# Kernel tuning notes

Hardware: AMD Instinct MI355X
Metric: run time of the kernel (lower is better)

The kernel has to match this reference:

```python
import jax, jax.numpy as jnp
import numpy as np

D = 128; H = 8; L = 6; DFF = 512; EPS = 1e-5; ETA = 1e-3; MAXLEN = 5000


def layernorm(x, g, b):
    m = jnp.mean(x, -1, keepdims=True)
    v = jnp.mean((x - m) ** 2, -1, keepdims=True)
    return (x - m) / jnp.sqrt(v + EPS) * g + b


def mha(q_in, kv_in, Wi, bi, Wo, bo):
    # Wi: [3D, D] packed q/k/v projections (torch in_proj layout)
    dh = D // H
    q = q_in @ Wi[:D].T + bi[:D]
    k = kv_in @ Wi[D:2 * D].T + bi[D:2 * D]
    v = kv_in @ Wi[2 * D:].T + bi[2 * D:]
    B_, Lq, _ = q.shape
    Lk = k.shape[1]
    q = q.reshape(B_, Lq, H, dh)
    k = k.reshape(B_, Lk, H, dh)
    v = v.reshape(B_, Lk, H, dh)
    att = jax.nn.softmax(jnp.einsum('bqhd,bkhd->bhqk', q, k) / jnp.sqrt(jnp.asarray(dh, q.dtype)), axis=-1)
    o = jnp.einsum('bhqk,bkhd->bqhd', att, v).reshape(B_, Lq, D)
    return o @ Wo.T + bo


def posenc(x):
    pos = jnp.arange(MAXLEN, dtype=x.dtype)[:, None]
    div = jnp.exp(jnp.arange(0, D, 2, dtype=x.dtype) * (-jnp.log(jnp.asarray(10000.0, x.dtype)) / D))
    pe = jnp.zeros((MAXLEN, D), x.dtype).at[:, 0::2].set(jnp.sin(pos * div)).at[:, 1::2].set(jnp.cos(pos * div))
    # faithful to original: slices pe by x.size(0) which is the BATCH dim (batch_first tensors)
    return x + pe[: x.shape[0], None, :]


def reference(src, tgt, emb, femb_w, femb_b,
              enc_inw, enc_inb, enc_ow, enc_ob, enc_l1g, enc_l1b, enc_l2g, enc_l2b,
              enc_f1w, enc_f1b, enc_f2w, enc_f2b, enc_ng, enc_nb,
              dec_inw, dec_inb, dec_ow, dec_ob, dec_cinw, dec_cinb, dec_cow, dec_cob,
              dec_l1g, dec_l1b, dec_l2g, dec_l2b, dec_l3g, dec_l3b,
              dec_f1w, dec_f1b, dec_f2w, dec_f2b, dec_ng, dec_nb, fc_w, fc_b):
    scale = jnp.sqrt(jnp.asarray(D, jnp.float32))
    s = posenc(emb[src] * scale)                     # [B,S,D]
    t = posenc((tgt @ femb_w.T + femb_b) * scale)    # [B,T,D]
    mem = s
    for i in range(L):  # encoder (post-norm, ReLU, dropout=0 in eval)
        a = mha(mem, mem, enc_inw[i], enc_inb[i], enc_ow[i], enc_ob[i])
        mem = layernorm(mem + a, enc_l1g[i], enc_l1b[i])
        f = jax.nn.relu(mem @ enc_f1w[i].T + enc_f1b[i]) @ enc_f2w[i].T + enc_f2b[i]
        mem = layernorm(mem + f, enc_l2g[i], enc_l2b[i])
    mem = layernorm(mem, enc_ng, enc_nb)
    y = t
    for i in range(L):  # decoder
        a = mha(y, y, dec_inw[i], dec_inb[i], dec_ow[i], dec_ob[i])
        y = layernorm(y + a, dec_l1g[i], dec_l1b[i])
        c = mha(y, mem, dec_cinw[i], dec_cinb[i], dec_cow[i], dec_cob[i])
        y = layernorm(y + c, dec_l2g[i], dec_l2b[i])
        f = jax.nn.relu(y @ dec_f1w[i].T + dec_f1b[i]) @ dec_f2w[i].T + dec_f2b[i]
        y = layernorm(y + f, dec_l3g[i], dec_l3b[i])
    y = layernorm(y, dec_ng, dec_nb)
    out = y @ fc_w.T + fc_b  # [B,T,1]
    # nn-corrected TN parameter vector: vec + eta * nn_output (pre-final-contract)
    return tgt[..., 0] + ETA * out[..., 0]


def setup_inputs():
    B, S, T = 4, 100, 2048
    ks = iter(jax.random.split(jax.random.key(0), 64))

    def w(shape, s=0.02):
        return jax.random.normal(next(ks), shape, jnp.float32) * s

    inp = {}
    inp['src'] = jax.random.randint(next(ks), (B, S), 0, 2)
    inp['tgt'] = jax.random.normal(next(ks), (B, T, 1), jnp.float32)
    inp['emb'] = w((2, D), 1.0)
    inp['femb_w'] = w((D, 1)); inp['femb_b'] = jnp.zeros((D,))
    inp['enc_inw'] = w((L, 3 * D, D)); inp['enc_inb'] = jnp.zeros((L, 3 * D))
    inp['enc_ow'] = w((L, D, D)); inp['enc_ob'] = jnp.zeros((L, D))
    inp['enc_l1g'] = jnp.ones((L, D)); inp['enc_l1b'] = jnp.zeros((L, D))
    inp['enc_l2g'] = jnp.ones((L, D)); inp['enc_l2b'] = jnp.zeros((L, D))
    inp['enc_f1w'] = w((L, DFF, D)); inp['enc_f1b'] = jnp.zeros((L, DFF))
    inp['enc_f2w'] = w((L, D, DFF)); inp['enc_f2b'] = jnp.zeros((L, D))
    inp['enc_ng'] = jnp.ones((D,)); inp['enc_nb'] = jnp.zeros((D,))
    inp['dec_inw'] = w((L, 3 * D, D)); inp['dec_inb'] = jnp.zeros((L, 3 * D))
    inp['dec_ow'] = w((L, D, D)); inp['dec_ob'] = jnp.zeros((L, D))
    inp['dec_cinw'] = w((L, 3 * D, D)); inp['dec_cinb'] = jnp.zeros((L, 3 * D))
    inp['dec_cow'] = w((L, D, D)); inp['dec_cob'] = jnp.zeros((L, D))
    inp['dec_l1g'] = jnp.ones((L, D)); inp['dec_l1b'] = jnp.zeros((L, D))
    inp['dec_l2g'] = jnp.ones((L, D)); inp['dec_l2b'] = jnp.zeros((L, D))
    inp['dec_l3g'] = jnp.ones((L, D)); inp['dec_l3b'] = jnp.zeros((L, D))
    inp['dec_f1w'] = w((L, DFF, D)); inp['dec_f1b'] = jnp.zeros((L, DFF))
    inp['dec_f2w'] = w((L, D, DFF)); inp['dec_f2b'] = jnp.zeros((L, D))
    inp['dec_ng'] = jnp.ones((D,)); inp['dec_nb'] = jnp.zeros((D,))
    inp['fc_w'] = w((1, D)); inp['fc_b'] = jnp.zeros((1,))
    return inp
```

## Files before the change

### kernel.cpp

```cpp
#include <hip/hip_runtime.h>
#include <hip/hip_bf16.h>
#include <math.h>

#define B_ 4
#define S_ 100
#define T_ 2048
#define DM 128
#define NH 8
#define DH 16
#define NL 6
#define DFFN 512

#define SQRT_D 11.313708498984761f
#define LN10K  9.210340371976184f
#define QSCALE 0.36067376022224085f

typedef _Float16 v4h __attribute__((ext_vector_type(4)));
typedef _Float16 v8h __attribute__((ext_vector_type(8)));
typedef float    v4f __attribute__((ext_vector_type(4)));

__device__ __forceinline__ float fexp2(float x) { return __builtin_amdgcn_exp2f(x); }

__device__ __forceinline__ v4f mfma16(v4h a, v4h b, v4f c) {
    return __builtin_amdgcn_mfma_f32_16x16x16f16(a, b, c, 0, 0, 0);
// ... 95 lines not shown
    v4f acc[4][2];
    #pragma unroll
    for (int m = 0; m < 4; m++)
        #pragma unroll
        for (int n = 0; n < 2; n++) acc[m][n] = (v4f){0.f, 0.f, 0.f, 0.f};

    for (int k0 = 0; k0 < K; k0 += 64) {
        #pragma unroll
        for (int i = 0; i < 4; i++) {
            int id = i * 256 + t;
            int r = id >> 3, j = id & 7;
            int gr = min(row0 + r, M - 1);
            int4 v = *(const int4*)(A + (size_t)gr * K + k0 + j * 8);
            *(int4*)&As[r][j * 8] = v;
        }
        #pragma unroll
        for (int i = 0; i < 2; i++) {
            int id = i * 256 + t;
            int r = id >> 3, j = id & 7;
            int4 v = *(const int4*)(W + (size_t)(col0 + r) * K + k0 + j * 8);
            *(int4*)&Ws[r][j * 8] = v;
        }
        __syncthreads();
        #pragma unroll
        for (int kk = 0; kk < 4; kk++) {
            v4h a[4], bf[2];
            #pragma unroll
            for (int m = 0; m < 4; m++)
                a[m] = *(const v4h*)&As[wrow0 + m * 16 + col16][kk * 16 + grp * 4];
            #pragma unroll
            for (int n = 0; n < 2; n++)
                bf[n] = *(const v4h*)&Ws[wcol0 + n * 16 + col16][kk * 16 + grp * 4];
            #pragma unroll
            for (int m = 0; m < 4; m++)
                #pragma unroll
                for (int n = 0; n < 2; n++)
                    acc[m][n] = mfma16(a[m], bf[n], acc[m][n]);
        }
        __syncthreads();
    }

    #pragma unroll
    for (int n = 0; n < 2; n++) {
        int gcol = col0 + wcol0 + n * 16 + col16;
        float bv = bias[gcol];
        #pragma unroll
        for (int m = 0; m < 4; m++) {
            int rbase = row0 + wrow0 + m * 16 + grp * 4;
            #pragma unroll
            for (int r = 0; r < 4; r++) {
                int grow = rbase + r;
                if (grow >= M) continue;
                float v = acc[m][n][r] + bv;
                if (MODE == 1) {
                    Ch[(size_t)grow * N + gcol] = (_Float16)fmaxf(v, 0.f);
                } else {
                    int pc = gcol + part_off;
                    int part = pc >> 7;
                    int h = (pc >> 4) & 7;
                    int d = pc & 15;
                    int b = Lshift ? (grow >> Lshift) : (grow / L);
                    int pos = grow - b * L;
                    int bh = b * NH + h;
                    if (part == 0)
                        qo[((size_t)bh * L + pos) * 16 + d] = (_Float16)(v * QSCALE);
                    else if (part == 1)
                        ko[((size_t)bh * L + pos) * 16 + d] = (_Float16)v;
                    else
                        vo[((size_t)bh * 16 + d) * Lkp + pos] = (_Float16)v;
                }
            }
        }
    }
}

template<int MERGE>
__global__ __launch_bounds__(128) void gemm_ln(
    const _Float16* __restrict__ A, const _Float16* __restrict__ W,
    const float* __restrict__ bias, const _Float16* __restrict__ res,
    const float* __restrict__ g, const float* __restrict__ bt,
    const _Float16* __restrict__ po, const float* __restrict__ pm, const float* __restrict__ pl,
    _Float16* __restrict__ youth, int M, int K)
{
    __shared__ _Float16 As[32][72];
    __shared__ _Float16 Ws[128][72];
    const int t = threadIdx.x;
    const int wave = t >> 6, lane = t & 63;
    const int col16 = lane & 15, grp = lane >> 4;
    const int row0 = blockIdx.x * 32;

    v4f acc[8];
    #pragma unroll
    for (int n = 0; n < 8; n++) acc[n] = (v4f){0.f, 0.f, 0.f, 0.f};

    for (int k0 = 0; k0 < K; k0 += 64) {
        #pragma unroll
        for (int i = 0; i < 2; i++) {
            int id = i * 128 + t;
            int r = id >> 3, j = id & 7;
            int grow = min(row0 + r, M - 1);
            if (MERGE) {
                int dim0 = k0 + j * 8;
                int h = dim0 >> 4;
                int doff = dim0 & 8;
                int b = grow >> 11, q = grow & 2047;
                size_t i0 = ((size_t)(b * 2 + 0) * NH + h) * T_ + q;
                size_t i1 = ((size_t)(b * 2 + 1) * NH + h) * T_ + q;
                float m0 = pm[i0], m1 = pm[i1];
                float MM = fmaxf(m0, m1);
                float w0 = fexp2(m0 - MM) * pl[i0];
                float w1 = fexp2(m1 - MM) * pl[i1];
                float inv = 1.0f / (w0 + w1);
                w0 *= inv; w1 *= inv;
                v8h o0 = *(const v8h*)&po[i0 * 16 + doff];
                v8h o1 = *(const v8h*)&po[i1 * 16 + doff];
                v8h mrg;
                #pragma unroll
                for (int e = 0; e < 8; e++)
                    mrg[e] = (_Float16)((float)o0[e] * w0 + (float)o1[e] * w1);
                *(v8h*)&As[r][j * 8] = mrg;
            } else {
                int4 v = *(const int4*)(A + (size_t)grow * K + k0 + j * 8);
                *(int4*)&As[r][j * 8] = v;
            }
        }
        #pragma unroll
        for (int i = 0; i < 8; i++) {
            int id = i * 128 + t;
            int r = id >> 3, j = id & 7;
            int4 v = *(const int4*)(W + (size_t)r * K + k0 + j * 8);
            *(int4*)&Ws[r][j * 8] = v;
        }
        __syncthreads();
        #pragma unroll
        for (int kk = 0; kk < 4; kk++) {
            v4h a = *(const v4h*)&As[wave * 16 + col16][kk * 16 + grp * 4];
            #pragma unroll
            for (int n = 0; n < 8; n++) {
                v4h bf = *(const v4h*)&Ws[n * 16 + col16][kk * 16 + grp * 4];
                acc[n] = mfma16(a, bf, acc[n]);
            }
        }
        __syncthreads();
    }

    float bv[8], gv[8], btv[8];
    #pragma unroll
    for (int n = 0; n < 8; n++) {
        bv[n]  = bias[col16 + 16 * n];
        gv[n]  = g[col16 + 16 * n];
        btv[n] = bt[col16 + 16 * n];
    }
    #pragma unroll
    for (int r = 0; r < 4; r++) {
        int row = row0 + wave * 16 + grp * 4 + r;
        if (row < M) {
            float x[8];
            float sum = 0.f;
            #pragma unroll
            for (int n = 0; n < 8; n++) {
                x[n] = acc[n][r] + bv[n] + (float)res[(size_t)row * DM + col16 + 16 * n];
                sum += x[n];
            }
            sum += __shfl_xor(sum, 1, 64);
            sum += __shfl_xor(sum, 2, 64);
            sum += __shfl_xor(sum, 4, 64);
            sum += __shfl_xor(sum, 8, 64);
            float mean = sum * (1.0f / 128.0f);
            float vs = 0.f;
            #pragma unroll
            for (int n = 0; n < 8; n++) {
                x[n] -= mean;
                vs += x[n] * x[n];
            }
            vs += __shfl_xor(vs, 1, 64);
            vs += __shfl_xor(vs, 2, 64);
            vs += __shfl_xor(vs, 4, 64);
            vs += __shfl_xor(vs, 8, 64);
            float rstd = rsqrtf(vs * (1.0f / 128.0f) + 1e-5f);
            #pragma unroll
            for (int n = 0; n < 8; n++) {
                float o = x[n] * rstd * gv[n] + btv[n];
                youth[(size_t)row * DM + col16 + 16 * n] = (_Float16)o;
            }
        }
    }
}

__global__ __launch_bounds__(128) void ffn_ln(
    const _Float16* __restrict__ A, const _Float16* __restrict__ W1,
    const float* __restrict__ b1, const _Float16* __restrict__ W2,
    const float* __restrict__ b2, const _Float16* __restrict__ res,
    const float* __restrict__ g, const float* __restrict__ bt,
    _Float16* __restrict__ youth, int M)
{
    __shared__ _Float16 As[32][136];
    __shared__ _Float16 W1s[64][136];
    __shared__ _Float16 Hs[32][72];
    __shared__ _Float16 W2s[128][72];
    const int t = threadIdx.x;
    const int wave = t >> 6, lane = t & 63;
    const int col16 = lane & 15, grp = lane >> 4;
    const int row0 = blockIdx.x * 32;

    #pragma unroll
    for (int rd = 0; rd < 4; rd++) {
        int id = rd * 128 + t;
        int r = id >> 4, j = id & 15;
        int grow = min(row0 + r, M - 1);
        int4 v = *(const int4*)(A + (size_t)grow * DM + j * 8);
        *(int4*)&As[r][j * 8] = v;
    }

    v4f oacc[8];
    #pragma unroll
    for (int n = 0; n < 8; n++) oacc[n] = (v4f){0.f, 0.f, 0.f, 0.f};
    __syncthreads();

    for (int hc = 0; hc < 8; hc++) {
        #pragma unroll
        for (int rd = 0; rd < 8; rd++) {
            int id = rd * 128 + t;
            int r = id >> 4, j = id & 15;
            int4 v = *(const int4*)(W1 + (size_t)(hc * 64 + r) * DM + j * 8);
            *(int4*)&W1s[r][j * 8] = v;
        }
        #pragma unroll
        for (int rd = 0; rd < 8; rd++) {
            int id = rd * 128 + t;
            int r = id >> 3, j = id & 7;
            int4 v = *(const int4*)(W2 + (size_t)r * DFFN + hc * 64 + j * 8);
            *(int4*)&W2s[r][j * 8] = v;
        }
        __syncthreads();
        v4f hacc[4];
        #pragma unroll
        for (int n = 0; n < 4; n++) hacc[n] = (v4f){0.f, 0.f, 0.f, 0.f};
        #pragma unroll
        for (int kk = 0; kk < 8; kk++) {
            v4h a = *(const v4h*)&As[wave * 16 + col16][kk * 16 + grp * 4];
            #pragma unroll
            for (int n = 0; n < 4; n++) {
                v4h bf = *(const v4h*)&W1s[n * 16 + col16][kk * 16 + grp * 4];
                hacc[n] = mfma16(a, bf, hacc[n]);
            }
        }
        #pragma unroll
        for (int n = 0; n < 4; n++) {
            float bb = b1[hc * 64 + n * 16 + col16];
            #pragma unroll
            for (int r = 0; r < 4; r++) {
                float h = fmaxf(hacc[n][r] + bb, 0.f);
                Hs[wave * 16 + grp * 4 + r][n * 16 + col16] = (_Float16)h;
            }
        }
        #pragma unroll
        for (int kk = 0; kk < 4; kk++) {
            v4h a = *(const v4h*)&Hs[wave * 16 + col16][kk * 16 + grp * 4];
            #pragma unroll
            for (int n = 0; n < 8; n++) {
                v4h bf = *(const v4h*)&W2s[n * 16 + col16][kk * 16 + grp * 4];
                oacc[n] = mfma16(a, bf, oacc[n]);
            }
        }
        __syncthreads();
    }

    float bv[8], gv[8], btv[8];
    #pragma unroll
    for (int n = 0; n < 8; n++) {
        bv[n]  = b2[col16 + 16 * n];
        gv[n]  = g[col16 + 16 * n];
        btv[n] = bt[col16 + 16 * n];
    }
    #pragma unroll
    for (int r = 0; r < 4; r++) {
        int row = row0 + wave * 16 + grp * 4 + r;
        if (row < M) {
            float x[8];
            float sum = 0.f;
            #pragma unroll
            for (int n = 0; n < 8; n++) {
                x[n] = oacc[n][r] + bv[n] + (float)res[(size_t)row * DM + col16 + 16 * n];
                sum += x[n];
            }
            sum += __shfl_xor(sum, 1, 64);
            sum += __shfl_xor(sum, 2, 64);
            sum += __shfl_xor(sum, 4, 64);
            sum += __shfl_xor(sum, 8, 64);
            float mean = sum * (1.0f / 128.0f);
            float vs = 0.f;
            #pragma unroll
            for (int n = 0; n < 8; n++) {
                x[n] -= mean;
                vs += x[n] * x[n];
            }
            vs += __shfl_xor(vs, 1, 64);
            vs += __shfl_xor(vs, 2, 64);
            vs += __shfl_xor(vs, 4, 64);
            vs += __shfl_xor(vs, 8, 64);
            float rstd = rsqrtf(vs * (1.0f / 128.0f) + 1e-5f);
            #pragma unroll
            for (int n = 0; n < 8; n++) {
                float o = x[n] * rstd * gv[n] + btv[n];
                youth[(size_t)row * DM + col16 + 16 * n] = (_Float16)o;
            }
        }
    }
}

__global__ __launch_bounds__(128) void cross_ln(
    const _Float16* __restrict__ y, const _Float16* __restrict__ Wq,
    const float* __restrict__ bq, const _Float16* __restrict__ KC_l,
    const _Float16* __restrict__ VC_l, const _Float16* __restrict__ Wo,
    const float* __restrict__ bo, const float* __restrict__ g,
    const float* __restrict__ bt, _Float16* __restrict__ youth)
{
    __shared__ _Float16 YO[32][136];
    __shared__ _Float16 Qs[32][136];
    __shared__ _Float16 Ws[128][72];
    __shared__ _Float16 Khs[128 * 16];
    __shared__ _Float16 Vhs[16 * 128];
    const int t = threadIdx.x;
    const int wave = t >> 6, lane = t & 63;
    const int col16 = lane & 15, grp = lane >> 4;
    const int row0 = blockIdx.x * 32;
    const int b = row0 >> 11;

    #pragma unroll
    for (int rd = 0; rd < 4; rd++) {
        int id = rd * 128 + t;
        int r = id >> 4, j = id & 15;
        int4 v = *(const int4*)(y + (size_t)(row0 + r) * DM + j * 8);
        *(int4*)&YO[r][j * 8] = v;
    }
    __syncthreads();

    {
        v4f qacc[8];
        #pragma unroll
        for (int n = 0; n < 8; n++) qacc[n] = (v4f){0.f, 0.f, 0.f, 0.f};
        for (int k0 = 0; k0 < 128; k0 += 64) {
            #pragma unroll
            for (int i = 0; i < 8; i++) {
                int id = i * 128 + t;
                int r = id >> 3, j = id & 7;
                int4 v = *(const int4*)(Wq + (size_t)r * DM + k0 + j * 8);
                *(int4*)&Ws[r][j * 8] = v;
            }
            __syncthreads();
            #pragma unroll
            for (int kk = 0; kk < 4; kk++) {
                v4h a = *(const v4h*)&YO[wave * 16 + col16][k0 + kk * 16 + grp * 4];
                #pragma unroll
                for (int n = 0; n < 8; n++) {
                    v4h bf = *(const v4h*)&Ws[n * 16 + col16][kk * 16 + grp * 4];
                    qacc[n] = mfma16(a, bf, qacc[n]);
                }
            }
            __syncthreads();
        }
        #pragma unroll
        for (int n = 0; n < 8; n++) {
            float bb = bq[n * 16 + col16];
            #pragma unroll
            for (int r = 0; r < 4; r++)
                Qs[wave * 16 + grp * 4 + r][n * 16 + col16] =
                    (_Float16)((qacc[n][r] + bb) * QSCALE);
        }
    }

    const char* kbB = (const char*)(KC_l + (size_t)(b * NH) * S_ * DH);
    const char* vbB = (const char*)(VC_l + (size_t)(b * NH) * DH * 128);
    for (int h = 0; h < NH; h++) {
        __syncthreads();
        #pragma unroll
        for (int rd = 0; rd < 2; rd++) {
            int dst = rd * 2048 + t * 16;
            int krow = (dst >> 5);
            int half = (t & 1);
            gload_lds16(kbB + (long)h * 3200 + (long)krow * 32 +
                        ((half ^ ((krow >> 2) & 1)) << 4),
                        (char*)Khs + rd * 2048);
        }
        #pragma unroll
        for (int rd = 0; rd < 2; rd++) {
            int dst = rd * 2048 + t * 16;
            int vd = dst >> 8;
            int inoff = (t & 15) * 16;
            gload_lds16(vbB + (long)h * 4096 + (long)vd * 256 +
                        (inoff ^ ((vd & 7) << 4)),
                        (char*)Vhs + rd * 2048);
        }
        __syncthreads();

        v4h q_frag = *(const v4h*)&Qs[wave * 16 + col16][h * 16 + grp * 4];
        const int kxor = (col16 & 4) << 2;
        v4f s4[7];
        #pragma unroll
        for (int sub = 0; sub < 7; sub++) {
            int koff = ((sub * 16 + col16) << 5) + ((grp * 8) ^ kxor);
            v4h k_frag = *(const v4h*)((const char*)Khs + koff);
            s4[sub] = mfma16(k_frag, q_frag, (v4f){0.f, 0.f, 0.f, 0.f});
        }
        #pragma unroll
        for (int r = 0; r < 4; r++) {
            int key = 96 + grp * 4 + r;
            if (key >= S_) s4[6][r] = -1e30f;
        }
        float mx = -1e30f;
        #pragma unroll
        for (int sub = 0; sub < 7; sub++)
            #pragma unroll
            for (int r = 0; r < 4; r++) mx = fmaxf(mx, s4[sub][r]);
        mx = fmaxf(mx, __shfl_xor(mx, 16, 64));
        mx = fmaxf(mx, __shfl_xor(mx, 32, 64));
        float l = 0.f;
        float p[7][4];
        #pragma unroll
        for (int sub = 0; sub < 7; sub++)
            #pragma unroll
            for (int r = 0; r < 4; r++) {
                p[sub][r] = fexp2(s4[sub][r] - mx);
                l += p[sub][r];
            }
        l += __shfl_xor(l, 16, 64);
        l += __shfl_xor(l, 32, 64);
        float inv = 1.0f / l;
        v4f o = {0.f, 0.f, 0.f, 0.f};
        #pragma unroll
        for (int sub = 0; sub < 7; sub++) {
            v4h ph = { (_Float16)(p[sub][0] * inv), (_Float16)(p[sub][1] * inv),
                       (_Float16)(p[sub][2] * inv), (_Float16)(p[sub][3] * inv) };
            int vbyte = (col16 << 8) + ((sub * 32 + grp * 8) ^ ((col16 & 7) << 4));
            v4h vt = *(const v4h*)((const char*)Vhs + vbyte);
            o = mfma16(vt, ph, o);
        }
        #pragma unroll
        for (int r = 0; r < 4; r++)
            YO[wave * 16 + col16][h * 16 + grp * 4 + r] = (_Float16)o[r];
    }
    __syncthreads();

    v4f acc[8];
    #pragma unroll
    for (int n = 0; n < 8; n++) acc[n] = (v4f){0.f, 0.f, 0.f, 0.f};
    for (int k0 = 0; k0 < 128; k0 += 64) {
        #pragma unroll
        for (int i = 0; i < 8; i++) {
            int id = i * 128 + t;
            int r = id >> 3, j = id & 7;
            int4 v = *(const int4*)(Wo + (size_t)r * DM + k0 + j * 8);
            *(int4*)&Ws[r][j * 8] = v;
        }
        __syncthreads();
        #pragma unroll
        for (int kk = 0; kk < 4; kk++) {
            v4h a = *(const v4h*)&YO[wave * 16 + col16][k0 + kk * 16 + grp * 4];
            #pragma unroll
            for (int n = 0; n < 8; n++) {
                v4h bf = *(const v4h*)&Ws[n * 16 + col16][kk * 16 + grp * 4];
                acc[n] = mfma16(a, bf, acc[n]);
            }
        }
        __syncthreads();
    }
    float bv[8], gv[8], btv[8];
    #pragma unroll
    for (int n = 0; n < 8; n++) {
        bv[n]  = bo[col16 + 16 * n];
        gv[n]  = g[col16 + 16 * n];
        btv[n] = bt[col16 + 16 * n];
    }
    #pragma unroll
    for (int r = 0; r < 4; r++) {
        int row = row0 + wave * 16 + grp * 4 + r;
        float x[8];
        float sum = 0.f;
        #pragma unroll
        for (int n = 0; n < 8; n++) {
            x[n] = acc[n][r] + bv[n] + (float)youth[(size_t)row * DM + col16 + 16 * n];
            sum += x[n];
        }
        sum += __shfl_xor(sum, 1, 64);
        sum += __shfl_xor(sum, 2, 64);
        sum += __shfl_xor(sum, 4, 64);
        sum += __shfl_xor(sum, 8, 64);
        float mean = sum * (1.0f / 128.0f);
        float vs = 0.f;
        #pragma unroll
        for (int n = 0; n < 8; n++) {
            x[n] -= mean;
            vs += x[n] * x[n];
        }
        vs += __shfl_xor(vs, 1, 64);
        vs += __shfl_xor(vs, 2, 64);
        vs += __shfl_xor(vs, 4, 64);
        vs += __shfl_xor(vs, 8, 64);
        float rstd = rsqrtf(vs * (1.0f / 128.0f) + 1e-5f);
        #pragma unroll
        for (int n = 0; n < 8; n++) {
            float oo = x[n] * rstd * gv[n] + btv[n];
            youth[(size_t)row * DM + col16 + 16 * n] = (_Float16)oo;
        }
    }
}

template<int FINAL>
__global__ __launch_bounds__(256, 6) void attn_p3(
    const _Float16* __restrict__ qh, const _Float16* __restrict__ kh,
    const _Float16* __restrict__ vth, _Float16* __restrict__ outh,
    _Float16* __restrict__ po, float* __restrict__ pm, float* __restrict__ pl,
    int Lq, int Lk, int Lkp, int NS)
{
    __shared__ _Float16 KV[2][2048];
    const int zb = blockIdx.z;
    const int b = zb / NS, split = zb - b * NS;
    const int h = blockIdx.y;
    const int wave = threadIdx.x >> 6, lane = threadIdx.x & 63;
    const int col16 = lane & 15, grp = lane >> 4;
    const int bh = b * NH + h;
    const int qrow = (blockIdx.x * 4 + wave) * 16 + col16;
    const int qcl = min(qrow, Lq - 1);

    v4h q_frag = *(const v4h*)(qh + ((size_t)bh * Lq + qcl) * 16 + grp * 4);
    const char* kbB = (const char*)(kh + (size_t)bh * Lk * 16);
    const char* vbB = (const char*)(vth + (size_t)bh * 16 * Lkp);
    const int LkpB = Lkp * 2;

    const int kvLen = Lk / NS;
    const int kv0 = split * kvLen;
    const int kvEnd = kv0 + kvLen;

    const int krow = wave * 32 + (lane >> 1);
    const long ksrc_off = (long)krow * 32 + (((lane & 1) ^ ((krow >> 2) & 1)) << 4);
    const int vd = (wave & 1) * 8 + (lane >> 3);
    const long vsrc_off = (long)vd * LkpB + (((lane & 7) * 16) ^ ((vd & 7) << 4));
    char* ldsK = (char*)&KV[0][0] + wave * 1024;
    char* ldsV = (char*)&KV[0][0] + 2048 + (wave & 1) * 1024;

    auto stage = [&](int buf, int kc) {
        if (wave < 2)
            gload_lds16(kbB + (long)kc * 32 + ksrc_off, ldsK + buf * 4096);
        else
            gload_lds16(vbB + (long)kc * 2 + vsrc_off, ldsV + buf * 4096);
    };

    const int kxor = (col16 & 4) << 2;

    float m = -1e30f;
    v4f l4 = {0.f, 0.f, 0.f, 0.f};
    v4f oa = {0.f, 0.f, 0.f, 0.f}, ob = {0.f, 0.f, 0.f, 0.f};

    stage(0, kv0);
    __syncthreads();

// ... 150 lines not shown
    const float* enc_nb  = (const float*)d_in[18];
    const float* dec_inw = (const float*)d_in[19];
    const float* dec_inb = (const float*)d_in[20];
    const float* dec_ow  = (const float*)d_in[21];
    const float* dec_ob  = (const float*)d_in[22];
    const float* dec_cinw= (const float*)d_in[23];
    const float* dec_cinb= (const float*)d_in[24];
    const float* dec_cow = (const float*)d_in[25];
    const float* dec_cob = (const float*)d_in[26];
    const float* dec_l1g = (const float*)d_in[27];
    const float* dec_l1b = (const float*)d_in[28];
    const float* dec_l2g = (const float*)d_in[29];
    const float* dec_l2b = (const float*)d_in[30];
    const float* dec_l3g = (const float*)d_in[31];
    const float* dec_l3b = (const float*)d_in[32];
    const float* dec_f1w = (const float*)d_in[33];
    const float* dec_f1b = (const float*)d_in[34];
    const float* dec_f2w = (const float*)d_in[35];
    const float* dec_f2b = (const float*)d_in[36];
    const float* dec_ng  = (const float*)d_in[37];
    const float* dec_nb  = (const float*)d_in[38];
    const float* fc_w    = (const float*)d_in[39];
    const float* fc_b    = (const float*)d_in[40];

    float* ws = (float*)d_ws;
    float* pm   = ws;
    float* pl   = ws + 131072;
    _Float16* hb = (_Float16*)(ws + 262144);
    _Float16* mem_h  = hb;
    _Float16* ybuf_h = hb + 51200;
    _Float16* aout_h = hb + 1099776;
    _Float16* wh     = hb + 2148352;
    _Float16* po     = hb + 4900864;
    _Float16* QH     = hb + 11192320;
    _Float16* KH     = hb + 12240896;
    _Float16* VTH    = hb + 13289472;
    _Float16* KC     = hb + 14338048;
    _Float16* VC     = hb + 14645248;

    const long W_ENC_INW = 0,       W_ENC_OW = 294912,  W_ENC_F1W = 393216,  W_ENC_F2W = 786432;
    const long W_DEC_INW = 1179648, W_DEC_OW = 1474560, W_DEC_CINW = 1572864, W_DEC_COW = 1867776;
    const long W_DEC_F1W = 1966080, W_DEC_F2W = 2359296;

    conv_w<<<dim3(384, 10), 256, 0, stream>>>(enc_inw, enc_ow, enc_f1w, enc_f2w,
                                              dec_inw, dec_ow, dec_cinw, dec_cow,
                                              dec_f1w, dec_f2w, wh);

    embed_src_kernel<<<200, 256, 0, stream>>>(src, emb, mem_h);
    for (int i = 0; i < NL; i++) {
        gemm_h<2><<<dim3(4, 6), 256, 0, stream>>>(mem_h, wh + W_ENC_INW + i * 49152, enc_inb + i * 384,
            nullptr, QH, KH, VTH, 400, 384, 128, 100, 128, 0, 0, 0, 0, 0, 0);
        attn_p3<1><<<dim3(2, NH, B_), 256, 0, stream>>>(QH, KH, VTH, aout_h,
            nullptr, nullptr, nullptr, 100, 100, 128, 1);
        gemm_ln<0><<<13, 128, 0, stream>>>(aout_h, wh + W_ENC_OW + i * 16384, enc_ob + i * 128,
            mem_h, enc_l1g + i * 128, enc_l1b + i * 128, nullptr, nullptr, nullptr, mem_h, 400, 128);
        ffn_ln<<<13, 128, 0, stream>>>(mem_h, wh + W_ENC_F1W + i * 65536, enc_f1b + i * 512,
            wh + W_ENC_F2W + i * 65536, enc_f2b + i * 128,
            mem_h, enc_l2g + i * 128, enc_l2b + i * 128, mem_h, 400);
    }
    ln_h<<<100, 256, 0, stream>>>(mem_h, enc_ng, enc_nb, 400);
    gemm_h<2><<<dim3(4, 2, 6), 256, 0, stream>>>(mem_h, wh + W_DEC_CINW + 16384, dec_cinb + 128,
        nullptr, nullptr, KC, VC, 400, 256, 128, 100, 128, 128, 0,
        49152, 384, 51200, 65536);

    embed_tgt_kernel<<<4096, 256, 0, stream>>>(tgt, femb_w, femb_b, ybuf_h);
    for (int i = 0; i < NL; i++) {
        gemm_h<2><<<dim3(64, 6), 256, 0, stream>>>(ybuf_h, wh + W_DEC_INW + i * 49152, dec_inb + i * 384,
            nullptr, QH, KH, VTH, 8192, 384, 128, 2048, 2048, 0, 11, 0, 0, 0, 0);
        attn_p3<0><<<dim3(32, NH, B_ * 2), 256, 0, stream>>>(QH, KH, VTH, nullptr,
            po, pm, pl, 2048, 2048, 2048, 2);
        gemm_ln<1><<<256, 128, 0, stream>>>(nullptr, wh + W_DEC_OW + i * 16384, dec_ob + i * 128,
            ybuf_h, dec_l1g + i * 128, dec_l1b + i * 128, po, pm, pl, ybuf_h, 8192, 128);
        cross_ln<<<256, 128, 0, stream>>>(ybuf_h, wh + W_DEC_CINW + i * 49152, dec_cinb + i * 384,
            KC + i * 51200, VC + i * 65536, wh + W_DEC_COW + i * 16384, dec_cob + i * 128,
            dec_l2g + i * 128, dec_l2b + i * 128, ybuf_h);
        ffn_ln<<<256, 128, 0, stream>>>(ybuf_h, wh + W_DEC_F1W + i * 65536, dec_f1b + i * 512,
            wh + W_DEC_F2W + i * 65536, dec_f2b + i * 128,
            ybuf_h, dec_l3g + i * 128, dec_l3b + i * 128, ybuf_h, 8192);
    }
    final_ln_kernel<<<2048, 256, 0, stream>>>(ybuf_h, tgt, dec_ng, dec_nb, fc_w, fc_b, (float*)d_out);
}
```

Before: 797.1 us.

## Fuse out-proj LN, cross-attention LN and FFN LN into one post-attention kernel

Merges three per-layer decoder kernels (self-attn output projection + LayerNorm, cross-attention block + LayerNorm, FFN + LayerNorm) into a single post_ln kernel that keeps the 32-row activation tile in shared memory between stages. The encoder likewise fuses out-proj+LN with FFN+LN. This removes two global round trips of the activation buffer and two launches per layer. In exchange the block needs much more shared memory, which lowers occupancy. The change also drops the Ch output path of gemm_h and changes the grid of the encoder cross-KV projection.

```diff
diff --git a/kernel.cpp b/kernel.cpp
--- a/kernel.cpp
+++ b/kernel.cpp
@@ -171,54 +171,65 @@
                 int grow = rbase + r;
                 if (grow >= M) continue;
                 float v = acc[m][n][r] + bv;
-                if (MODE == 1) {
-                    Ch[(size_t)grow * N + gcol] = (_Float16)fmaxf(v, 0.f);
-                } else {
-                    int pc = gcol + part_off;
-                    int part = pc >> 7;
-                    int h = (pc >> 4) & 7;
-                    int d = pc & 15;
-                    int b = Lshift ? (grow >> Lshift) : (grow / L);
-                    int pos = grow - b * L;
-                    int bh = b * NH + h;
-                    if (part == 0)
-                        qo[((size_t)bh * L + pos) * 16 + d] = (_Float16)(v * QSCALE);
-                    else if (part == 1)
-                        ko[((size_t)bh * L + pos) * 16 + d] = (_Float16)v;
-                    else
-                        vo[((size_t)bh * 16 + d) * Lkp + pos] = (_Float16)v;
-                }
-            }
-        }
-    }
-}
-
-template<int MERGE>
-__global__ __launch_bounds__(128) void gemm_ln(
-    const _Float16* __restrict__ A, const _Float16* __restrict__ W,
-    const float* __restrict__ bias, const _Float16* __restrict__ res,
-    const float* __restrict__ g, const float* __restrict__ bt,
+                int pc = gcol + part_off;
+                int part = pc >> 7;
+                int h = (pc >> 4) & 7;
+                int d = pc & 15;
+                int b = Lshift ? (grow >> Lshift) : (grow / L);
+                int pos = grow - b * L;
+                int bh = b * NH + h;
+                if (part == 0)
+                    qo[((size_t)bh * L + pos) * 16 + d] = (_Float16)(v * QSCALE);
+                else if (part == 1)
+                    ko[((size_t)bh * L + pos) * 16 + d] = (_Float16)v;
+                else
+                    vo[((size_t)bh * 16 + d) * Lkp + pos] = (_Float16)v;
+            }
+        }
+    }
+}
+
+template<int CROSS>
+__global__ __launch_bounds__(128) void post_ln(
+    const _Float16* __restrict__ A,
     const _Float16* __restrict__ po, const float* __restrict__ pm, const float* __restrict__ pl,
-    _Float16* __restrict__ youth, int M, int K)
+    const _Float16* __restrict__ Wo1, const float* __restrict__ bo1,
+    const _Float16* __restrict__ resg,
+    const float* __restrict__ g1, const float* __restrict__ bt1,
+    const _Float16* __restrict__ Wq, const float* __restrict__ bq,
+    const _Float16* __restrict__ KC_l, const _Float16* __restrict__ VC_l,
+    const _Float16* __restrict__ Wo2, const float* __restrict__ bo2,
+    const float* __restrict__ g2, const float* __restrict__ bt2,
+    const _Float16* __restrict__ W1, const float* __restrict__ fb1,
+    const _Float16* __restrict__ W2, const float* __restrict__ fb2,
+    const float* __restrict__ g3, const float* __restrict__ bt3,
+    _Float16* __restrict__ yout, int M)
 {
     __shared__ _Float16 As[32][72];
     __shared__ _Float16 Ws[128][72];
+    __shared__ _Float16 YL[32][136];
+    __shared__ _Float16 QS[32][136];
+    __shared__ _Float16 Khs[2048];
+    __shared__ _Float16 Vhs[2048];
+    __shared__ _Float16 W1s[64][136];
+    __shared__ _Float16 Hs[32][72];
+    __shared__ _Float16 W2s[128][72];
     const int t = threadIdx.x;
     const int wave = t >> 6, lane = t & 63;
     const int col16 = lane & 15, grp = lane >> 4;
     const int row0 = blockIdx.x * 32;
+    const int rl = wave * 16 + grp * 4;
 
     v4f acc[8];
     #pragma unroll
     for (int n = 0; n < 8; n++) acc[n] = (v4f){0.f, 0.f, 0.f, 0.f};
-
-    for (int k0 = 0; k0 < K; k0 += 64) {
+    for (int k0 = 0; k0 < 128; k0 += 64) {
         #pragma unroll
         for (int i = 0; i < 2; i++) {
             int id = i * 128 + t;
             int r = id >> 3, j = id & 7;
             int grow = min(row0 + r, M - 1);
-            if (MERGE) {
+            if (CROSS) {
                 int dim0 = k0 + j * 8;
                 int h = dim0 >> 4;
                 int doff = dim0 & 8;
@@ -239,7 +250,7 @@
                     mrg[e] = (_Float16)((float)o0[e] * w0 + (float)o1[e] * w1);
                 *(v8h*)&As[r][j * 8] = mrg;
             } else {
-                int4 v = *(const int4*)(A + (size_t)grow * K + k0 + j * 8);
+                int4 v = *(const int4*)(A + (size_t)grow * DM + k0 + j * 8);
                 *(int4*)&As[r][j * 8] = v;
             }
         }
@@ -247,7 +258,7 @@
         for (int i = 0; i < 8; i++) {
             int id = i * 128 + t;
             int r = id >> 3, j = id & 7;
-            int4 v = *(const int4*)(W + (size_t)r * K + k0 + j * 8);
+            int4 v = *(const int4*)(Wo1 + (size_t)r * DM + k0 + j * 8);
             *(int4*)&Ws[r][j * 8] = v;
         }
         __syncthreads();
@@ -262,23 +273,26 @@
         }
         __syncthreads();
     }
-
-    float bv[8], gv[8], btv[8];
-    #pragma unroll
-    for (int n = 0; n < 8; n++) {
-        bv[n]  = bias[col16 + 16 * n];
-        gv[n]  = g[col16 + 16 * n];
-        btv[n] = bt[col16 + 16 * n];
-    }
-    #pragma unroll
-    for (int r = 0; r < 4; r++) {
-        int row = row0 + wave * 16 + grp * 4 + r;
-        if (row < M) {
+    {
+        float bv[8], gv[8], btv[8];
+        #pragma unroll
+        for (int n = 0; n < 8; n++) {
+            bv[n] = bo1[col16 + 16 * n];
+            gv[n] = g1[col16 + 16 * n];
+            btv[n] = bt1[col16 + 16 * n];
+        }
+        #pragma unroll
+        for (int r = 0; r < 4; r++) {
+            int grow = min(row0 + rl + r, M - 1);
             float x[8];
             float sum = 0.f;
             #pragma unroll
             for (int n = 0; n < 8; n++) {
-                x[n] = acc[n][r] + bv[n] + (float)res[(size_t)row * DM + col16 + 16 * n];
+                x[n] = acc[r == 0 ? 0 : 0][0] * 0.f;
+            }
+            #pragma unroll
+            for (int n = 0; n < 8; n++) {
+                x[n] = acc[n][r] + bv[n] + (float)resg[(size_t)grow * DM + col16 + 16 * n];
                 sum += x[n];
             }
             sum += __shfl_xor(sum, 1, 64);
@@ -288,54 +302,188 @@
             float mean = sum * (1.0f / 128.0f);
             float vs = 0.f;
             #pragma unroll
-            for (int n = 0; n < 8; n++) {
-                x[n] -= mean;
-                vs += x[n] * x[n];
-            }
+            for (int n = 0; n < 8; n++) { x[n] -= mean; vs += x[n] * x[n]; }
             vs += __shfl_xor(vs, 1, 64);
             vs += __shfl_xor(vs, 2, 64);
             vs += __shfl_xor(vs, 4, 64);
             vs += __shfl_xor(vs, 8, 64);
             float rstd = rsqrtf(vs * (1.0f / 128.0f) + 1e-5f);
             #pragma unroll
+            for (int n = 0; n < 8; n++)
+                YL[rl + r][col16 + 16 * n] = (_Float16)(x[n] * rstd * gv[n] + btv[n]);
+        }
+    }
+    __syncthreads();
+
+    if (CROSS) {
+        v4f qacc[8];
+        #pragma unroll
+        for (int n = 0; n < 8; n++) qacc[n] = (v4f){0.f, 0.f, 0.f, 0.f};
+        for (int k0 = 0; k0 < 128; k0 += 64) {
+            #pragma unroll
+            for (int i = 0; i < 8; i++) {
+                int id = i * 128 + t;
+                int r = id >> 3, j = id & 7;
+                int4 v = *(const int4*)(Wq + (size_t)r * DM + k0 + j * 8);
+                *(int4*)&Ws[r][j * 8] = v;
+            }
+            __syncthreads();
+            #pragma unroll
+            for (int kk = 0; kk < 4; kk++) {
+                v4h a = *(const v4h*)&YL[wave * 16 + col16][k0 + kk * 16 + grp * 4];
+                #pragma unroll
+                for (int n = 0; n < 8; n++) {
+                    v4h bf = *(const v4h*)&Ws[n * 16 + col16][kk * 16 + grp * 4];
+                    qacc[n] = mfma16(a, bf, qacc[n]);
+                }
+            }
+            __syncthreads();
+        }
+        #pragma unroll
+        for (int n = 0; n < 8; n++) {
+            float bb = bq[n * 16 + col16];
+            #pragma unroll
+            for (int r = 0; r < 4; r++)
+                QS[rl + r][n * 16 + col16] = (_Float16)((qacc[n][r] + bb) * QSCALE);
+        }
+
+        const int b = row0 >> 11;
+        const char* kbB = (const char*)(KC_l + (size_t)(b * NH) * S_ * DH);
+        const char* vbB = (const char*)(VC_l + (size_t)(b * NH) * DH * 128);
+        for (int h = 0; h < NH; h++) {
+            __syncthreads();
+            #pragma unroll
+            for (int rd = 0; rd < 2; rd++) {
+                int dstB = rd * 2048 + wave * 1024 + lane * 16;
+                int krow = dstB >> 5;
+                int half = (dstB >> 4) & 1;
+                gload_lds16(kbB + (long)h * 3200 + (long)krow * 32 +
+                            ((half ^ ((krow >> 2) & 1)) << 4),
+                            (char*)Khs + rd * 2048 + wave * 1024);
+            }
+            #pragma unroll
+            for (int rd = 0; rd < 2; rd++) {
+                int dstB = rd * 2048 + wave * 1024 + lane * 16;
+                int vd = dstB >> 8;
+                int inoff = dstB & 255;
+                gload_lds16(vbB + (long)h * 4096 + (long)vd * 256 +
+                            (inoff ^ ((vd & 7) << 4)),
+                            (char*)Vhs + rd * 2048 + wave * 1024);
+            }
+            __syncthreads();
+
+            v4h q_frag = *(const v4h*)&QS[wave * 16 + col16][h * 16 + grp * 4];
+            const int kxor = (col16 & 4) << 2;
+            v4f s4[7];
+            #pragma unroll
+            for (int sub = 0; sub < 7; sub++) {
+                int koff = ((sub * 16 + col16) << 5) + ((grp * 8) ^ kxor);
+                v4h k_frag = *(const v4h*)((const char*)Khs + koff);
+                s4[sub] = mfma16(k_frag, q_frag, (v4f){0.f, 0.f, 0.f, 0.f});
+            }
+            #pragma unroll
+            for (int r = 0; r < 4; r++) {
+                int key = 96 + grp * 4 + r;
+                if (key >= S_) s4[6][r] = -1e30f;
+            }
+            float mx = -1e30f;
+            #pragma unroll
+            for (int sub = 0; sub < 7; sub++)
+                #pragma unroll
+                for (int r = 0; r < 4; r++) mx = fmaxf(mx, s4[sub][r]);
+            mx = fmaxf(mx, __shfl_xor(mx, 16, 64));
+            mx = fmaxf(mx, __shfl_xor(mx, 32, 64));
+            float l = 0.f;
+            float p[7][4];
+            #pragma unroll
+            for (int sub = 0; sub < 7; sub++)
+                #pragma unroll
+                for (int r = 0; r < 4; r++) {
+                    p[sub][r] = fexp2(s4[sub][r] - mx);
+                    l += p[sub][r];
+                }
+            l += __shfl_xor(l, 16, 64);
+            l += __shfl_xor(l, 32, 64);
+            float inv = 1.0f / l;
+            v4f o = {0.f, 0.f, 0.f, 0.f};
+            #pragma unroll
+            for (int sub = 0; sub < 7; sub++) {
+                v4h ph = { (_Float16)(p[sub][0] * inv), (_Float16)(p[sub][1] * inv),
+                           (_Float16)(p[sub][2] * inv), (_Float16)(p[sub][3] * inv) };
+                int vbyte = (col16 << 8) + ((sub * 32 + grp * 8) ^ ((col16 & 7) << 4));
+                v4h vt = *(const v4h*)((const char*)Vhs + vbyte);
+                o = mfma16(vt, ph, o);
+            }
+            #pragma unroll
+            for (int r = 0; r < 4; r++)
+                QS[wave * 16 + col16][h * 16 + grp * 4 + r] = (_Float16)o[r];
+        }
+        __syncthreads();
+
+        v4f ac2[8];
+        #pragma unroll
+        for (int n = 0; n < 8; n++) ac2[n] = (v4f){0.f, 0.f, 0.f, 0.f};
+        for (int k0 = 0; k0 < 128; k0 += 64) {
+            #pragma unroll
+            for (int i = 0; i < 8; i++) {
+                int id = i * 128 + t;
+                int r = id >> 3, j = id & 7;
+                int4 v = *(const int4*)(Wo2 + (size_t)r * DM + k0 + j * 8);
+                *(int4*)&Ws[r][j * 8] = v;
+            }
+            __syncthreads();
+            #pragma unroll
+            for (int kk = 0; kk < 4; kk++) {
+                v4h a = *(const v4h*)&QS[wave * 16 + col16][k0 + kk * 16 + grp * 4];
+                #pragma unroll
+                for (int n = 0; n < 8; n++) {
+                    v4h bf = *(const v4h*)&Ws[n * 16 + col16][kk * 16 + grp * 4];
+                    ac2[n] = mfma16(a, bf, ac2[n]);
+                }
+            }
+            __syncthreads();
+        }
+        {
+            float bv[8], gv[8], btv[8];
+            #pragma unroll
             for (int n = 0; n < 8; n++) {
-                float o = x[n] * rstd * gv[n] + btv[n];
-                youth[(size_t)row * DM + col16 + 16 * n] = (_Float16)o;
-            }
-        }
-    }
-}
-
-__global__ __launch_bounds__(128) void ffn_ln(
-    const _Float16* __restrict__ A, const _Float16* __restrict__ W1,
-    const float* __restrict__ b1, const _Float16* __restrict__ W2,
-    const float* __restrict__ b2, const _Float16* __restrict__ res,
-    const float* __restrict__ g, const float* __restrict__ bt,
-    _Float16* __restrict__ youth, int M)
-{
-    __shared__ _Float16 As[32][136];
-    __shared__ _Float16 W1s[64][136];
-    __shared__ _Float16 Hs[32][72];
-    __shared__ _Float16 W2s[128][72];
-    const int t = threadIdx.x;
-    const int wave = t >> 6, lane = t & 63;
-    const int col16 = lane & 15, grp = lane >> 4;
-    const int row0 = blockIdx.x * 32;
-
-    #pragma unroll
-    for (int rd = 0; rd < 4; rd++) {
-        int id = rd * 128 + t;
-        int r = id >> 4, j = id & 15;
-        int grow = min(row0 + r, M - 1);
-        int4 v = *(const int4*)(A + (size_t)grow * DM + j * 8);
-        *(int4*)&As[r][j * 8] = v;
+                bv[n] = bo2[col16 + 16 * n];
+                gv[n] = g2[col16 + 16 * n];
+                btv[n] = bt2[col16 + 16 * n];
+            }
+            #pragma unroll
+            for (int r = 0; r < 4; r++) {
+                float x[8];
+                float sum = 0.f;
+                #pragma unroll
+                for (int n = 0; n < 8; n++) {
+                    x[n] = ac2[n][r] + bv[n] + (float)YL[rl + r][col16 + 16 * n];
+                    sum += x[n];
+                }
+                sum += __shfl_xor(sum, 1, 64);
+                sum += __shfl_xor(sum, 2, 64);
+                sum += __shfl_xor(sum, 4, 64);
+                sum += __shfl_xor(sum, 8, 64);
+                float mean = sum * (1.0f / 128.0f);
+                float vs = 0.f;
+                #pragma unroll
+                for (int n = 0; n < 8; n++) { x[n] -= mean; vs += x[n] * x[n]; }
+                vs += __shfl_xor(vs, 1, 64);
+                vs += __shfl_xor(vs, 2, 64);
+                vs += __shfl_xor(vs, 4, 64);
+                vs += __shfl_xor(vs, 8, 64);
+                float rstd = rsqrtf(vs * (1.0f / 128.0f) + 1e-5f);
+                #pragma unroll
+                for (int n = 0; n < 8; n++)
+                    YL[rl + r][col16 + 16 * n] = (_Float16)(x[n] * rstd * gv[n] + btv[n]);
+            }
+        }
+        __syncthreads();
     }
 
     v4f oacc[8];
     #pragma unroll
     for (int n = 0; n < 8; n++) oacc[n] = (v4f){0.f, 0.f, 0.f, 0.f};
-    __syncthreads();
-
     for (int hc = 0; hc < 8; hc++) {
         #pragma unroll
         for (int rd = 0; rd < 8; rd++) {
@@ -357,7 +505,7 @@
         for (int n = 0; n < 4; n++) hacc[n] = (v4f){0.f, 0.f, 0.f, 0.f};
         #pragma unroll
         for (int kk = 0; kk < 8; kk++) {
-            v4h a = *(const v4h*)&As[wave * 16 + col16][kk * 16 + grp * 4];
+            v4h a = *(const v4h*)&YL[wave * 16 + col16][kk * 16 + grp * 4];
             #pragma unroll
             for (int n = 0; n < 4; n++) {
                 v4h bf = *(const v4h*)&W1s[n * 16 + col16][kk * 16 + grp * 4];
@@ -366,11 +514,11 @@
         }
         #pragma unroll
         for (int n = 0; n < 4; n++) {
-            float bb = b1[hc * 64 + n * 16 + col16];
+            float bb = fb1[hc * 64 + n * 16 + col16];
             #pragma unroll
             for (int r = 0; r < 4; r++) {
                 float h = fmaxf(hacc[n][r] + bb, 0.f);
-                Hs[wave * 16 + grp * 4 + r][n * 16 + col16] = (_Float16)h;
+                Hs[rl + r][n * 16 + col16] = (_Float16)h;
             }
         }
         #pragma unroll
@@ -384,23 +532,22 @@
         }
         __syncthreads();
     }
-
-    float bv[8], gv[8], btv[8];
-    #pragma unroll
-    for (int n = 0; n < 8; n++) {
-        bv[n]  = b2[col16 + 16 * n];
-        gv[n]  = g[col16 + 16 * n];
-        btv[n] = bt[col16 + 16 * n];
-    }
-    #pragma unroll
-    for (int r = 0; r < 4; r++) {
-        int row = row0 + wave * 16 + grp * 4 + r;
-        if (row < M) {
+    {
+        float bv[8], gv[8], btv[8];
+        #pragma unroll
+        for (int n = 0; n < 8; n++) {
+            bv[n] = fb2[col16 + 16 * n];
+            gv[n] = g3[col16 + 16 * n];
+            btv[n] = bt3[col16 + 16 * n];
+        }
+        #pragma unroll
+        for (int r = 0; r < 4; r++) {
+            int row = row0 + rl + r;
             float x[8];
             float sum = 0.f;
             #pragma unroll
             for (int n = 0; n < 8; n++) {
-                x[n] = oacc[n][r] + bv[n] + (float)res[(size_t)row * DM + col16 + 16 * n];
+                x[n] = oacc[n][r] + bv[n] + (float)YL[rl + r][col16 + 16 * n];
                 sum += x[n];
             }
             sum += __shfl_xor(sum, 1, 64);
@@ -410,217 +557,19 @@
             float mean = sum * (1.0f / 128.0f);
             float vs = 0.f;
             #pragma unroll
-            for (int n = 0; n < 8; n++) {
-                x[n] -= mean;
-                vs += x[n] * x[n];
-            }
+            for (int n = 0; n < 8; n++) { x[n] -= mean; vs += x[n] * x[n]; }
             vs += __shfl_xor(vs, 1, 64);
             vs += __shfl_xor(vs, 2, 64);
             vs += __shfl_xor(vs, 4, 64);
             vs += __shfl_xor(vs, 8, 64);
             float rstd = rsqrtf(vs * (1.0f / 128.0f) + 1e-5f);
-            #pragma unroll
-            for (int n = 0; n < 8; n++) {
-                float o = x[n] * rstd * gv[n] + btv[n];
-                youth[(size_t)row * DM + col16 + 16 * n] = (_Float16)o;
-            }
-        }
-    }
-}
-
-__global__ __launch_bounds__(128) void cross_ln(
-    const _Float16* __restrict__ y, const _Float16* __restrict__ Wq,
-    const float* __restrict__ bq, const _Float16* __restrict__ KC_l,
-    const _Float16* __restrict__ VC_l, const _Float16* __restrict__ Wo,
-    const float* __restrict__ bo, const float* __restrict__ g,
-    const float* __restrict__ bt, _Float16* __restrict__ youth)
-{
-    __shared__ _Float16 YO[32][136];
-    __shared__ _Float16 Qs[32][136];
-    __shared__ _Float16 Ws[128][72];
-    __shared__ _Float16 Khs[128 * 16];
-    __shared__ _Float16 Vhs[16 * 128];
-    const int t = threadIdx.x;
-    const int wave = t >> 6, lane = t & 63;
-    const int col16 = lane & 15, grp = lane >> 4;
-    const int row0 = blockIdx.x * 32;
-    const int b = row0 >> 11;
-
-    #pragma unroll
-    for (int rd = 0; rd < 4; rd++) {
-        int id = rd * 128 + t;
-        int r = id >> 4, j = id & 15;
-        int4 v = *(const int4*)(y + (size_t)(row0 + r) * DM + j * 8);
-        *(int4*)&YO[r][j * 8] = v;
-    }
-    __syncthreads();
-
-    {
-        v4f qacc[8];
-        #pragma unroll
-        for (int n = 0; n < 8; n++) qacc[n] = (v4f){0.f, 0.f, 0.f, 0.f};
-        for (int k0 = 0; k0 < 128; k0 += 64) {
-            #pragma unroll
-            for (int i = 0; i < 8; i++) {
-                int id = i * 128 + t;
-                int r = id >> 3, j = id & 7;
-                int4 v = *(const int4*)(Wq + (size_t)r * DM + k0 + j * 8);
-                *(int4*)&Ws[r][j * 8] = v;
-            }
-            __syncthreads();
-            #pragma unroll
-            for (int kk = 0; kk < 4; kk++) {
-                v4h a = *(const v4h*)&YO[wave * 16 + col16][k0 + kk * 16 + grp * 4];
+            if (row < M) {
                 #pragma unroll
                 for (int n = 0; n < 8; n++) {
-                    v4h bf = *(const v4h*)&Ws[n * 16 + col16][kk * 16 + grp * 4];
-                    qacc[n] = mfma16(a, bf, qacc[n]);
+                    float o = x[n] * rstd * gv[n] + btv[n];
+                    yout[(size_t)row * DM + col16 + 16 * n] = (_Float16)o;
                 }
             }
-            __syncthreads();
-        }
-        #pragma unroll
-        for (int n = 0; n < 8; n++) {
-            float bb = bq[n * 16 + col16];
-            #pragma unroll
-            for (int r = 0; r < 4; r++)
-                Qs[wave * 16 + grp * 4 + r][n * 16 + col16] =
-                    (_Float16)((qacc[n][r] + bb) * QSCALE);
-        }
-    }
-
-    const char* kbB = (const char*)(KC_l + (size_t)(b * NH) * S_ * DH);
-    const char* vbB = (const char*)(VC_l + (size_t)(b * NH) * DH * 128);
-    for (int h = 0; h < NH; h++) {
-        __syncthreads();
-        #pragma unroll
-        for (int rd = 0; rd < 2; rd++) {
-            int dst = rd * 2048 + t * 16;
-            int krow = (dst >> 5);
-            int half = (t & 1);
-            gload_lds16(kbB + (long)h * 3200 + (long)krow * 32 +
-                        ((half ^ ((krow >> 2) & 1)) << 4),
-                        (char*)Khs + rd * 2048);
-        }
-        #pragma unroll
-        for (int rd = 0; rd < 2; rd++) {
-            int dst = rd * 2048 + t * 16;
-            int vd = dst >> 8;
-            int inoff = (t & 15) * 16;
-            gload_lds16(vbB + (long)h * 4096 + (long)vd * 256 +
-                        (inoff ^ ((vd & 7) << 4)),
-                        (char*)Vhs + rd * 2048);
-        }
-        __syncthreads();
-
-        v4h q_frag = *(const v4h*)&Qs[wave * 16 + col16][h * 16 + grp * 4];
-        const int kxor = (col16 & 4) << 2;
-        v4f s4[7];
-        #pragma unroll
-        for (int sub = 0; sub < 7; sub++) {
-            int koff = ((sub * 16 + col16) << 5) + ((grp * 8) ^ kxor);
-            v4h k_frag = *(const v4h*)((const char*)Khs + koff);
-            s4[sub] = mfma16(k_frag, q_frag, (v4f){0.f, 0.f, 0.f, 0.f});
-        }
-        #pragma unroll
-        for (int r = 0; r < 4; r++) {
-            int key = 96 + grp * 4 + r;
-            if (key >= S_) s4[6][r] = -1e30f;
-        }
-        float mx = -1e30f;
-        #pragma unroll
-        for (int sub = 0; sub < 7; sub++)
-            #pragma unroll
-            for (int r = 0; r < 4; r++) mx = fmaxf(mx, s4[sub][r]);
-        mx = fmaxf(mx, __shfl_xor(mx, 16, 64));
-        mx = fmaxf(mx, __shfl_xor(mx, 32, 64));
-        float l = 0.f;
-        float p[7][4];
-        #pragma unroll
-        for (int sub = 0; sub < 7; sub++)
-            #pragma unroll
-            for (int r = 0; r < 4; r++) {
-                p[sub][r] = fexp2(s4[sub][r] - mx);
-                l += p[sub][r];
-            }
-        l += __shfl_xor(l, 16, 64);
-        l += __shfl_xor(l, 32, 64);
-        float inv = 1.0f / l;
-        v4f o = {0.f, 0.f, 0.f, 0.f};
-        #pragma unroll
-        for (int sub = 0; sub < 7; sub++) {
-            v4h ph = { (_Float16)(p[sub][0] * inv), (_Float16)(p[sub][1] * inv),
-                       (_Float16)(p[sub][2] * inv), (_Float16)(p[sub][3] * inv) };
-            int vbyte = (col16 << 8) + ((sub * 32 + grp * 8) ^ ((col16 & 7) << 4));
-            v4h vt = *(const v4h*)((const char*)Vhs + vbyte);
-            o = mfma16(vt, ph, o);
-        }
-        #pragma unroll
-        for (int r = 0; r < 4; r++)
-            YO[wave * 16 + col16][h * 16 + grp * 4 + r] = (_Float16)o[r];
-    }
-    __syncthreads();
-
-    v4f acc[8];
-    #pragma unroll
-    for (int n = 0; n < 8; n++) acc[n] = (v4f){0.f, 0.f, 0.f, 0.f};
-    for (int k0 = 0; k0 < 128; k0 += 64) {
-        #pragma unroll
-        for (int i = 0; i < 8; i++) {
-            int id = i * 128 + t;
-            int r = id >> 3, j = id & 7;
-            int4 v = *(const int4*)(Wo + (size_t)r * DM + k0 + j * 8);
-            *(int4*)&Ws[r][j * 8] = v;
-        }
-        __syncthreads();
-        #pragma unroll
-        for (int kk = 0; kk < 4; kk++) {
-            v4h a = *(const v4h*)&YO[wave * 16 + col16][k0 + kk * 16 + grp * 4];
-            #pragma unroll
-            for (int n = 0; n < 8; n++) {
-                v4h bf = *(const v4h*)&Ws[n * 16 + col16][kk * 16 + grp * 4];
-                acc[n] = mfma16(a, bf, acc[n]);
-            }
-        }
-        __syncthreads();
-    }
-    float bv[8], gv[8], btv[8];
-    #pragma unroll
-    for (int n = 0; n < 8; n++) {
-        bv[n]  = bo[col16 + 16 * n];
-        gv[n]  = g[col16 + 16 * n];
-        btv[n] = bt[col16 + 16 * n];
-    }
-    #pragma unroll
-    for (int r = 0; r < 4; r++) {
-        int row = row0 + wave * 16 + grp * 4 + r;
-        float x[8];
-        float sum = 0.f;
-        #pragma unroll
-        for (int n = 0; n < 8; n++) {
-            x[n] = acc[n][r] + bv[n] + (float)youth[(size_t)row * DM + col16 + 16 * n];
-            sum += x[n];
-        }
-        sum += __shfl_xor(sum, 1, 64);
-        sum += __shfl_xor(sum, 2, 64);
-        sum += __shfl_xor(sum, 4, 64);
-        sum += __shfl_xor(sum, 8, 64);
-        float mean = sum * (1.0f / 128.0f);
-        float vs = 0.f;
-        #pragma unroll
-        for (int n = 0; n < 8; n++) {
-            x[n] -= mean;
-            vs += x[n] * x[n];
-        }
-        vs += __shfl_xor(vs, 1, 64);
-        vs += __shfl_xor(vs, 2, 64);
-        vs += __shfl_xor(vs, 4, 64);
-        vs += __shfl_xor(vs, 8, 64);
-        float rstd = rsqrtf(vs * (1.0f / 128.0f) + 1e-5f);
-        #pragma unroll
-        for (int n = 0; n < 8; n++) {
-            float oo = x[n] * rstd * gv[n] + btv[n];
-            youth[(size_t)row * DM + col16 + 16 * n] = (_Float16)oo;
         }
     }
 }
@@ -877,14 +826,18 @@
             nullptr, QH, KH, VTH, 400, 384, 128, 100, 128, 0, 0, 0, 0, 0, 0);
         attn_p3<1><<<dim3(2, NH, B_), 256, 0, stream>>>(QH, KH, VTH, aout_h,
             nullptr, nullptr, nullptr, 100, 100, 128, 1);
-        gemm_ln<0><<<13, 128, 0, stream>>>(aout_h, wh + W_ENC_OW + i * 16384, enc_ob + i * 128,
-            mem_h, enc_l1g + i * 128, enc_l1b + i * 128, nullptr, nullptr, nullptr, mem_h, 400, 128);
-        ffn_ln<<<13, 128, 0, stream>>>(mem_h, wh + W_ENC_F1W + i * 65536, enc_f1b + i * 512,
+        post_ln<0><<<13, 128, 0, stream>>>(aout_h,
+            nullptr, nullptr, nullptr,
+            wh + W_ENC_OW + i * 16384, enc_ob + i * 128,
+            mem_h, enc_l1g + i * 128, enc_l1b + i * 128,
+            nullptr, nullptr, nullptr, nullptr, nullptr, nullptr, nullptr, nullptr,
+            wh + W_ENC_F1W + i * 65536, enc_f1b + i * 512,
             wh + W_ENC_F2W + i * 65536, enc_f2b + i * 128,
-            mem_h, enc_l2g + i * 128, enc_l2b + i * 128, mem_h, 400);
+            enc_l2g + i * 128, enc_l2b + i * 128,
+            mem_h, 400);
     }
     ln_h<<<100, 256, 0, stream>>>(mem_h, enc_ng, enc_nb, 400);
-    gemm_h<2><<<dim3(4, 2, 6), 256, 0, stream>>>(mem_h, wh + W_DEC_CINW + 16384, dec_cinb + 128,
+    gemm_h<2><<<dim3(4, 4, 6), 256, 0, stream>>>(mem_h, wh + W_DEC_CINW + 16384, dec_cinb + 128,
         nullptr, nullptr, KC, VC, 400, 256, 128, 100, 128, 128, 0,
         49152, 384, 51200, 65536);
 
@@ -894,14 +847,18 @@
             nullptr, QH, KH, VTH, 8192, 384, 128, 2048, 2048, 0, 11, 0, 0, 0, 0);
         attn_p3<0><<<dim3(32, NH, B_ * 2), 256, 0, stream>>>(QH, KH, VTH, nullptr,
             po, pm, pl, 2048, 2048, 2048, 2);
-        gemm_ln<1><<<256, 128, 0, stream>>>(nullptr, wh + W_DEC_OW + i * 16384, dec_ob + i * 128,
-            ybuf_h, dec_l1g + i * 128, dec_l1b + i * 128, po, pm, pl, ybuf_h, 8192, 128);
-        cross_ln<<<256, 128, 0, stream>>>(ybuf_h, wh + W_DEC_CINW + i * 49152, dec_cinb + i * 384,
-            KC + i * 51200, VC + i * 65536, wh + W_DEC_COW + i * 16384, dec_cob + i * 128,
-            dec_l2g + i * 128, dec_l2b + i * 128, ybuf_h);
-        ffn_ln<<<256, 128, 0, stream>>>(ybuf_h, wh + W_DEC_F1W + i * 65536, dec_f1b + i * 512,
+        post_ln<1><<<256, 128, 0, stream>>>(nullptr,
+            po, pm, pl,
+            wh + W_DEC_OW + i * 16384, dec_ob + i * 128,
+            ybuf_h, dec_l1g + i * 128, dec_l1b + i * 128,
+            wh + W_DEC_CINW + i * 49152, dec_cinb + i * 384,
+            KC + i * 51200, VC + i * 65536,
+            wh + W_DEC_COW + i * 16384, dec_cob + i * 128,
+            dec_l2g + i * 128, dec_l2b + i * 128,
+            wh + W_DEC_F1W + i * 65536, dec_f1b + i * 512,
             wh + W_DEC_F2W + i * 65536, dec_f2b + i * 128,
-            ybuf_h, dec_l3g + i * 128, dec_l3b + i * 128, ybuf_h, 8192);
+            dec_l3g + i * 128, dec_l3b + i * 128,
+            ybuf_h, 8192);
     }
     final_ln_kernel<<<2048, 256, 0, stream>>>(ybuf_h, tgt, dec_ng, dec_nb, fc_w, fc_b, (float*)d_out);
 }
```

Result: faster. 720.5 us (-9.6%).
